# Optimization experiments

Hardware: AMD Instinct MI355X
Metric: run time of the kernel (lower is better)

Reference implementation:

```python
import math
import jax, jax.numpy as jnp
import numpy as np

B, S, DIM = 1, 1024, 2048
H, KVH, HD = 16, 4, 128
HID, L, VOCAB = 8192, 2, 32000
NIMG, TOK_START = 256, 1
IMG_IN = 2 * 14 * 14 * 3  # temporal_patch*spatial_patch^2*channels
EPS = 1e-6


def _rms(x, w=None, eps=EPS):
    y = x * jax.lax.rsqrt(jnp.mean(x * x, axis=-1, keepdims=True) + eps)
    return y if w is None else y * w


def _rope(x, angles):
    # x: [B,S,H,D], angles: [S, D//2] pairwise rotation angles (3D RoPE: 1D+2D concat)
    c = jnp.cos(angles)[None, :, None, :]
    s = jnp.sin(angles)[None, :, None, :]
    x1, x2 = x[..., 0::2], x[..., 1::2]
    return jnp.stack([x1 * c - x2 * s, x1 * s + x2 * c], axis=-1).reshape(x.shape)


def setup_inputs() -> dict:
    key = jax.random.key(0)
    ks = jax.random.split(key, 12)
    sc = 0.02
    return {
        "tokens": jax.random.randint(ks[0], (B, S), 0, VOCAB),
        "img_feats": jax.random.normal(ks[1], (B, NIMG, IMG_IN), jnp.float32),
        "freqs_cis": jax.random.normal(ks[2], (S, HD // 4), jnp.float32),
        "freqs_cis_2d": jax.random.normal(ks[3], (S, HD // 4), jnp.float32),
        "tok_emb": jax.random.normal(ks[4], (VOCAB, DIM), jnp.float32) * sc,
        "img_proj_w": jax.random.normal(ks[5], (DIM, IMG_IN), jnp.float32) * sc,
        "wqkv": jax.random.normal(ks[6], (L, H * HD + 2 * KVH * HD, DIM), jnp.float32) * sc,
        "wo": jax.random.normal(ks[7], (L, DIM, H * HD), jnp.float32) * sc,
        "sinks": jax.random.normal(ks[8], (L, H), jnp.float32),
        "w13": jax.random.normal(ks[9], (L, 2 * HID, DIM), jnp.float32) * sc,
        "w2": jax.random.normal(ks[10], (L, DIM, HID), jnp.float32) * sc,
        "norm_w": jnp.ones((DIM,), jnp.float32),
        "output_w": jax.random.normal(ks[11], (VOCAB, DIM), jnp.float32) * sc,
    }


def reference(tokens, img_feats, freqs_cis, freqs_cis_2d, tok_emb, img_proj_w,
              wqkv, wo, sinks, w13, w2, norm_w, output_w):
    # token embeddings + slice-based scatter of projected image tokens
    x = tok_emb[tokens]                                   # [B,S,DIM]
    img = jnp.einsum('bnf,df->bnd', img_feats, img_proj_w)
    x = jax.lax.dynamic_update_slice(x, img, (0, TOK_START, 0))

    angles = jnp.concatenate([freqs_cis, freqs_cis_2d], axis=-1)  # [S, HD//2]
    scale = 1.0 / math.sqrt(HD)
    neg = jnp.where(jnp.tril(jnp.ones((S, S), bool)), 0.0, -jnp.inf)  # causal
    n_rep = H // KVH
    q_dim, kv_dim = H * HD, KVH * HD

    for i in range(L):
        # attention: RMSNorm -> QKV -> QK-norm -> GQA expand -> RoPE -> SDPA+lse
        h = _rms(x)
        qkv = h @ wqkv[i].T
        q = qkv[..., :q_dim].reshape(B, S, H, HD)
        k = qkv[..., q_dim:q_dim + kv_dim].reshape(B, S, KVH, HD)
        v = qkv[..., q_dim + kv_dim:].reshape(B, S, KVH, HD)
        q, k = _rms(q), _rms(k)
        k = jnp.repeat(k, n_rep, axis=2)  # repeat_interleave over kv heads
        v = jnp.repeat(v, n_rep, axis=2)
        q, k = _rope(q, angles), _rope(k, angles)
        scores = jnp.einsum('bqhd,bkhd->bhqk', q, k) * scale + neg
        lse = jax.nn.logsumexp(scores, axis=-1)            # [B,H,S]
        attn = jnp.exp(scores - lse[..., None])
        out = jnp.einsum('bhqk,bkhd->bqhd', attn, v)        # [B,S,H,HD]
        sink_scale = jax.nn.sigmoid(lse - sinks[i][None, :, None])  # [B,H,S]
        out = out * sink_scale.transpose(0, 2, 1)[..., None]
        x = x + out.reshape(B, S, H * HD) @ wo[i].T

        # FFN: RMSNorm -> interleaved gate/up -> relu(gate)^2 * up -> down
        h = _rms(x)
        packed = h @ w13[i].T
        gate, up = packed[..., 0::2], packed[..., 1::2]
        x = x + (jnp.square(jax.nn.relu(gate)) * up) @ w2[i].T

    return _rms(x, norm_w) @ output_w.T                    # [B,S,VOCAB]
```

## Files before the change

kernel.cpp:

```cpp
#include <hip/hip_runtime.h>

typedef __bf16 bf16;
typedef bf16 bf16x8 __attribute__((ext_vector_type(8)));
typedef bf16 bf16x4 __attribute__((ext_vector_type(4)));
typedef bf16 bf16x2 __attribute__((ext_vector_type(2)));
typedef float f32x4 __attribute__((ext_vector_type(4)));
typedef float f32x2 __attribute__((ext_vector_type(2)));

#define S_LEN 1024
#define DIM 2048
#define NH 16
#define NKVH 4
#define HD 128
#define HID 8192
#define VOCAB 32000
#define QKV_N 3072
#define W13_N 16384
#define IMG_K 1176
#define NIMG 256

#define AS1 __attribute__((address_space(1)))
#define AS3 __attribute__((address_space(3)))

__device__ inline f32x4 mfma16(bf16x8 a, bf16x8 b, f32x4 c) {
  return __builtin_amdgcn_mfma_f32_16x16x32_bf16(a, b, c, 0, 0, 0);
}

__global__ void embed_kernel(const int* __restrict__ tok, const float* __restrict__ emb,
                             float* __restrict__ x) {
  int s = blockIdx.x, t = threadIdx.x;
  int id = tok[s];
  const float* er = emb + (size_t)id * DIM;
  float* xr = x + (size_t)s * DIM;
  *(f32x4*)(xr + t * 8)     = *(const f32x4*)(er + t * 8);
  *(f32x4*)(xr + t * 8 + 4) = *(const f32x4*)(er + t * 8 + 4);
}

__global__ void cvt_kernel(const float* __restrict__ in, bf16* __restrict__ o, int n) {
  int i = blockIdx.x * 256 + threadIdx.x;
  if (i < n) o[i] = (bf16)in[i];
}
__global__ void cvt4_kernel(const float* __restrict__ in, bf16* __restrict__ o, int n4) {
  int i = blockIdx.x * 256 + threadIdx.x;
  if (i < n4) {
    f32x4 v = *(const f32x4*)(in + (size_t)i * 4);
    bf16x4 b;
    b[0] = (bf16)v[0]; b[1] = (bf16)v[1]; b[2] = (bf16)v[2]; b[3] = (bf16)v[3];
    *(bf16x4*)(o + (size_t)i * 4) = b;
  }
}

template<int USE_W>
__global__ void rmsnorm_kernel(const float* __restrict__ x, const float* __restrict__ w,
                               bf16* __restrict__ o) {
  const int row = blockIdx.x, t = threadIdx.x;
  const float* xr = x + (size_t)row * DIM;
  f32x4 a = *(const f32x4*)(xr + t * 8);
  f32x4 b = *(const f32x4*)(xr + t * 8 + 4);
  float ss = a[0]*a[0] + a[1]*a[1] + a[2]*a[2] + a[3]*a[3]
           + b[0]*b[0] + b[1]*b[1] + b[2]*b[2] + b[3]*b[3];
#pragma unroll
  for (int off = 1; off < 64; off <<= 1) ss += __shfl_xor(ss, off);
  __shared__ float red[4];
  if ((t & 63) == 0) red[t >> 6] = ss;
  __syncthreads();
  ss = red[0] + red[1] + red[2] + red[3];
  float r = rsqrtf(ss * (1.0f / DIM) + 1e-6f);
  bf16x8 ov;
  if (USE_W) {
    f32x4 w1 = *(const f32x4*)(w + t * 8);
    f32x4 w2v = *(const f32x4*)(w + t * 8 + 4);
    ov[0] = (bf16)(a[0]*r*w1[0]); ov[1] = (bf16)(a[1]*r*w1[1]);
    ov[2] = (bf16)(a[2]*r*w1[2]); ov[3] = (bf16)(a[3]*r*w1[3]);
    ov[4] = (bf16)(b[0]*r*w2v[0]); ov[5] = (bf16)(b[1]*r*w2v[1]);
    ov[6] = (bf16)(b[2]*r*w2v[2]); ov[7] = (bf16)(b[3]*r*w2v[3]);
  } else {
    ov[0] = (bf16)(a[0]*r); ov[1] = (bf16)(a[1]*r);
    ov[2] = (bf16)(a[2]*r); ov[3] = (bf16)(a[3]*r);
    ov[4] = (bf16)(b[0]*r); ov[5] = (bf16)(b[1]*r);
    ov[6] = (bf16)(b[2]*r); ov[7] = (bf16)(b[3]*r);
  }
  *(bf16x8*)(o + (size_t)row * DIM + t * 8) = ov;
}

__global__ void qkvpost_kernel(const float* __restrict__ qkv, const float* __restrict__ f1,
                               const float* __restrict__ f2, bf16* __restrict__ qb,
                               bf16* __restrict__ kb, bf16* __restrict__ vtb) {
  int s = blockIdx.x, t = threadIdx.x;
  __shared__ float cs[64], sn[64];
  if (t < 64) {
    float ang = (t < 32) ? f1[(size_t)s * 32 + t] : f2[(size_t)s * 32 + (t - 32)];
    cs[t] = cosf(ang);
    sn[t] = sinf(ang);
  }
  __syncthreads();
  int w = t >> 6, lane = t & 63;
  for (int hh = w; hh < 24; hh += 4) {
    const float* base = qkv + (size_t)s * QKV_N + hh * HD;
    f32x2 e = *(const f32x2*)(base + lane * 2);
    if (hh < 20) {
      float ssum = e[0]*e[0] + e[1]*e[1];
#pragma unroll
      for (int off = 1; off < 64; off <<= 1) ssum += __shfl_xor(ssum, off);
      float r = rsqrtf(ssum * (1.0f / HD) + 1e-6f);
      float x1 = e[0] * r, x2 = e[1] * r;
      float c = cs[lane], s2 = sn[lane];
      bf16x2 ov;
      ov[0] = (bf16)(x1 * c - x2 * s2);
      ov[1] = (bf16)(x1 * s2 + x2 * c);
      if (hh < 16)
        *(bf16x2*)(qb + ((size_t)hh * S_LEN + s) * HD + lane * 2) = ov;
      else
        *(bf16x2*)(kb + ((size_t)(hh - 16) * S_LEN + s) * HD + lane * 2) = ov;
    } else {
      int kv = hh - 20;
      vtb[((size_t)kv * HD + lane * 2) * S_LEN + s]     = (bf16)e[0];
      vtb[((size_t)kv * HD + lane * 2 + 1) * S_LEN + s] = (bf16)e[1];
    }
  }
}

__global__ __launch_bounds__(256) void attn_kernel(const bf16* __restrict__ qb,
                                                   const bf16* __restrict__ kb,
                                                   const bf16* __restrict__ vtb,
                                                   const float* __restrict__ sinks,
                                                   bf16* __restrict__ out) {
  const int h = blockIdx.y, qs = blockIdx.x;
  const int w = threadIdx.x >> 6, lane = threadIdx.x & 63;
  const int lo = lane & 15, hi = lane >> 4;
  const int q0 = qs * 16;
  const int q = q0 + lo;
  const int kvh = h >> 2;
  const bf16* Q = qb + (size_t)h * S_LEN * HD;
  const bf16* Kp = kb + (size_t)kvh * S_LEN * HD;
  const bf16* Vt = vtb + (size_t)kvh * HD * S_LEN;
  const float scale = 0.08838834764831845f;

  __shared__ float accS[4][64 * 36];
  __shared__ float mS[4][16], lS[4][16];

  bf16x8 qf[4];
#pragma unroll
  for (int ks = 0; ks < 4; ++ks)
    qf[ks] = *(const bf16x8*)(Q + (size_t)q * HD + ks * 32 + hi * 8);

  f32x4 accT[8];
#pragma unroll
  for (int i = 0; i < 8; ++i) accT[i] = (f32x4){0.f, 0.f, 0.f, 0.f};
  float mrow = -3e38f, lrow = 0.f;

  const int nt = (q0 + 15) / 32 + 1;
  for (int tile = w; tile < nt; tile += 4) {
    const int kv0 = tile * 32;
    f32x4 st0 = (f32x4){0.f,0.f,0.f,0.f}, st1 = (f32x4){0.f,0.f,0.f,0.f};
#pragma unroll
    for (int ks = 0; ks < 4; ++ks) {
      const bf16* kbase = Kp + (size_t)(kv0 + lo) * HD + ks * 32 + hi * 8;
      bf16x8 k0f = *(const bf16x8*)(kbase);
      bf16x8 k1f = *(const bf16x8*)(kbase + 16 * HD);
      st0 = mfma16(k0f, qf[ks], st0);
      st1 = mfma16(k1f, qf[ks], st1);
    }
    float p[2][4];
    float pmax = -3e38f;
#pragma unroll
    for (int r = 0; r < 4; ++r) {
      int kvg0 = kv0 + hi * 4 + r;
      float v0 = (kvg0 <= q) ? st0[r] * scale : -3e38f;
      int kvg1 = kvg0 + 16;
      float v1 = (kvg1 <= q) ? st1[r] * scale : -3e38f;
      p[0][r] = v0; p[1][r] = v1;
      pmax = fmaxf(pmax, fmaxf(v0, v1));
    }
    pmax = fmaxf(pmax, __shfl_xor(pmax, 16));
    pmax = fmaxf(pmax, __shfl_xor(pmax, 32));
    float mnew = fmaxf(mrow, pmax);
    float alpha = __expf(mrow - mnew);
    float ps = 0.f;
#pragma unroll
    for (int f = 0; f < 2; ++f)
#pragma unroll
      for (int r = 0; r < 4; ++r) {
        float e = __expf(p[f][r] - mnew);
        p[f][r] = e;
        ps += e;
      }
    ps += __shfl_xor(ps, 16);
    ps += __shfl_xor(ps, 32);
    lrow = lrow * alpha + ps;
    mrow = mnew;
#pragma unroll
    for (int fd = 0; fd < 8; ++fd) {
      accT[fd][0] *= alpha; accT[fd][1] *= alpha;
      accT[fd][2] *= alpha; accT[fd][3] *= alpha;
    }
    bf16x8 pb;
#pragma unroll
    for (int j = 0; j < 8; ++j) {
      int src = ((j >> 2) + 2 * (hi & 1)) * 16 + lo;
      float v0 = __shfl(p[0][j & 3], src);
      float v1 = __shfl(p[1][j & 3], src);
      pb[j] = (bf16)((hi >= 2) ? v1 : v0);
    }
#pragma unroll
    for (int fd = 0; fd < 8; ++fd) {
      bf16x8 vf = *(const bf16x8*)(Vt + (size_t)(fd * 16 + lo) * S_LEN + kv0 + hi * 8);
      accT[fd] = mfma16(vf, pb, accT[fd]);
    }
  }
  if (hi == 0) { mS[w][lo] = mrow; lS[w][lo] = lrow; }
  float* as = &accS[w][lane * 36];
#pragma unroll
  for (int fd = 0; fd < 8; ++fd) *(f32x4*)(as + fd * 4) = accT[fd];
  __syncthreads();
  float m0 = mS[0][lo], m1 = mS[1][lo], m2 = mS[2][lo], m3 = mS[3][lo];
  float mstar = fmaxf(fmaxf(m0, m1), fmaxf(m2, m3));
  float e0 = __expf(m0 - mstar), e1 = __expf(m1 - mstar);
  float e2 = __expf(m2 - mstar), e3 = __expf(m3 - mstar);
  float lstar = lS[0][lo]*e0 + lS[1][lo]*e1 + lS[2][lo]*e2 + lS[3][lo]*e3;
  float lse = mstar + __logf(lstar);
  float ssig = 1.f / (1.f + __expf(sinks[h] - lse));
  float sc = ssig / lstar;
#pragma unroll
  for (int f2 = 0; f2 < 2; ++f2) {
    int fd = w * 2 + f2;
    f32x4 a0 = *(const f32x4*)&accS[0][lane * 36 + fd * 4];
    f32x4 a1 = *(const f32x4*)&accS[1][lane * 36 + fd * 4];
    f32x4 a2 = *(const f32x4*)&accS[2][lane * 36 + fd * 4];
    f32x4 a3 = *(const f32x4*)&accS[3][lane * 36 + fd * 4];
#pragma unroll
    for (int r = 0; r < 4; ++r) {
      float o = a0[r]*e0 + a1[r]*e1 + a2[r]*e2 + a3[r]*e3;
      out[(size_t)q * DIM + h * HD + fd * 16 + hi * 4 + r] = (bf16)(o * sc);
    }
  }
}

__device__ inline void xcd_remap(int ntm, int ntn, int& mtile, int& ntile) {
  const int flat = blockIdx.x + ntm * blockIdx.y;
  const int chunk = ntm * 8;
  const int gfull = ntn >> 3;
  const int g = flat / chunk;
  if (g < gfull) {
    int rem = flat - g * chunk;
    ntile = g * 8 + (rem & 7);
    mtile = rem >> 3;
  } else {
    int rem = flat - gfull * chunk;
    int nrem = ntn - gfull * 8;
    ntile = gfull * 8 + rem % nrem;
    mtile = rem / nrem;
  }
}

enum { EPI_STORE = 0, EPI_ADD = 1, EPI_ACT = 2 };

template<int BM, int BN, int EPI, int GL>
__global__ void gemm_bt(const bf16* __restrict__ A, const float* __restrict__ W,
                        float* __restrict__ C, bf16* __restrict__ Cb,
                        int M, int N, int K, int ldc) {
  constexpr int BK = 64;
  __shared__ __align__(16) char lds[(BM + BN) * BK * 2];
  char* ldsA = lds;
  char* ldsB = lds + BM * BK * 2;
  const int t = threadIdx.x;
  int mtile, ntile;
  xcd_remap(gridDim.x, gridDim.y, mtile, ntile);
  const int m0 = mtile * BM, n0 = ntile * BN;

  const int wid = t >> 6, lane = t & 63;
  const int lo = lane & 15, hi = lane >> 4;
  const int wr = wid >> 1, wc = wid & 1;
  constexpr int TM = BM / 32, TN = BN / 32;
  constexpr int NA = BM / 32;
  constexpr int NPASS = BM / 32;
  constexpr int NW = BN / 16;

  f32x4 acc[TM][TN];
#pragma unroll
  for (int m = 0; m < TM; ++m)
#pragma unroll
    for (int n = 0; n < TN; ++n) acc[m][n] = (f32x4){0.f, 0.f, 0.f, 0.f};

  const int nk = (K + BK - 1) / BK;
  for (int kt = 0; kt < nk; ++kt) {
    const int k0 = kt * BK;
    bf16x8 av[NA];
    f32x4 wv[NW];
    if (!GL) {
#pragma unroll
      for (int i = 0; i < NA; ++i) {
        int c = t + i * 256;
        int row = c >> 3, kc = c & 7;
        int kg = k0 + kc * 8;
        bf16x8 z = {};
        av[i] = (kg < K) ? *(const bf16x8*)(A + (size_t)(m0 + row) * K + kg) : z;
      }
    }
#pragma unroll
    for (int i = 0; i < NW; ++i) {
      int c = t + i * 256;
      int row = c >> 4, kc = c & 15;
      int kg = k0 + kc * 4;
      f32x4 z = (f32x4){0.f, 0.f, 0.f, 0.f};
      wv[i] = (kg < K) ? *(const f32x4*)(W + (size_t)(n0 + row) * K + kg) : z;
    }
    __syncthreads();
    if (GL) {
#pragma unroll
      for (int i = 0; i < NPASS; ++i) {
        int row = i * 32 + (t >> 3);
        int srcb = ((t & 7) * 16) ^ ((row & 7) << 4);
        const bf16* g2 = A + (size_t)(m0 + row) * K + k0 + (srcb >> 1);
        char* l = ldsA + i * 4096 + wid * 1024;
        __builtin_amdgcn_global_load_lds((const AS1 void*)g2, (AS3 void*)l, 16, 0, 0);
      }
    } else {
#pragma unroll
      for (int i = 0; i < NA; ++i) {
        int c = t + i * 256;
        int row = c >> 3, kc = c & 7;
        int kb = (kc * 16) ^ ((row & 7) << 4);
        *(bf16x8*)(ldsA + row * 128 + kb) = av[i];
      }
    }
#pragma unroll
    for (int i = 0; i < NW; ++i) {
      int c = t + i * 256;
      int row = c >> 4, kc = c & 15;
      bf16x4 bv;
      bv[0] = (bf16)wv[i][0]; bv[1] = (bf16)wv[i][1];
      bv[2] = (bf16)wv[i][2]; bv[3] = (bf16)wv[i][3];
      int kb = (kc * 8) ^ ((row & 7) << 4);
      *(bf16x4*)(ldsB + row * 128 + kb) = bv;
    }
    __syncthreads();
#pragma unroll
    for (int ks = 0; ks < 2; ++ks) {
      bf16x8 af[TM], bfr[TN];
      int kbb = ks * 64 + hi * 16;
#pragma unroll
      for (int m = 0; m < TM; ++m) {
        int row = wr * (BM / 2) + m * 16 + lo;
        af[m] = *(const bf16x8*)(ldsA + row * 128 + (kbb ^ ((row & 7) << 4)));
      }
#pragma unroll
      for (int n = 0; n < TN; ++n) {
        int row = wc * (BN / 2) + n * 16 + lo;
        bfr[n] = *(const bf16x8*)(ldsB + row * 128 + (kbb ^ ((row & 7) << 4)));
      }
#pragma unroll
      for (int m = 0; m < TM; ++m)
#pragma unroll
        for (int n = 0; n < TN; ++n)
          acc[m][n] = mfma16(af[m], bfr[n], acc[m][n]);
    }
    __syncthreads();
  }
#pragma unroll
  for (int m = 0; m < TM; ++m) {
    int gmb = m0 + wr * (BM / 2) + m * 16 + hi * 4;
#pragma unroll
    for (int n = 0; n < TN; ++n) {
      int gn = n0 + wc * (BN / 2) + n * 16 + lo;
#pragma unroll
      for (int r = 0; r < 4; ++r) {
        float v = acc[m][n][r];
        if (EPI == EPI_STORE) {
          C[(size_t)(gmb + r) * ldc + gn] = v;
        } else if (EPI == EPI_ADD) {
          C[(size_t)(gmb + r) * ldc + gn] += v;
        } else {
          float pv = __shfl_xor(v, 1);
          if (!(lane & 1)) {
            float g2 = fmaxf(v, 0.f);
            Cb[(size_t)(gmb + r) * (W13_N / 2) + (gn >> 1)] = (bf16)(g2 * g2 * pv);
          }
        }
      }
    }
  }
}

template<int BM, int BN, int EPI>
__global__ __launch_bounds__(256) void gemm_bb(const bf16* __restrict__ A,
                                               const bf16* __restrict__ W,
                                               float* __restrict__ C, bf16* __restrict__ Cb,
                                               int K, int ldc) {
  constexpr int BK = 64;
  __shared__ __align__(16) char lds[(BM + BN) * BK * 2];
  char* ldsA = lds;
  char* ldsB = lds + BM * BK * 2;
  const int t = threadIdx.x;
  int mtile, ntile;
  xcd_remap(gridDim.x, gridDim.y, mtile, ntile);
  const int m0 = mtile * BM, n0 = ntile * BN;

  const int wid = t >> 6, lane = t & 63;
  const int lo = lane & 15, hi = lane >> 4;
  const int wr = wid >> 1, wc = wid & 1;
  constexpr int TM = BM / 32, TN = BN / 32;
  constexpr int PA = BM / 32, PB = BN / 32;

  f32x4 acc[TM][TN];
#pragma unroll
  for (int m = 0; m < TM; ++m)
#pragma unroll
    for (int n = 0; n < TN; ++n) acc[m][n] = (f32x4){0.f, 0.f, 0.f, 0.f};

  const int prow = t >> 3;
  const int psrcb = (t & 7) * 16;
  const int nk = K / BK;
  for (int kt = 0; kt < nk; ++kt) {
    const int k0 = kt * BK;
#pragma unroll
    for (int i = 0; i < PA; ++i) {
      int row = i * 32 + prow;
      int srcb = psrcb ^ ((row & 7) << 4);
      const bf16* g = A + (size_t)(m0 + row) * K + k0 + (srcb >> 1);
      __builtin_amdgcn_global_load_lds((const AS1 void*)g,
                                       (AS3 void*)(ldsA + i * 4096 + wid * 1024), 16, 0, 0);
    }
#pragma unroll
    for (int i = 0; i < PB; ++i) {
      int row = i * 32 + prow;
      int srcb = psrcb ^ ((row & 7) << 4);
      const bf16* g = W + (size_t)(n0 + row) * K + k0 + (srcb >> 1);
      __builtin_amdgcn_global_load_lds((const AS1 void*)g,
                                       (AS3 void*)(ldsB + i * 4096 + wid * 1024), 16, 0, 0);
    }
    __syncthreads();
#pragma unroll
    for (int ks = 0; ks < 2; ++ks) {
      bf16x8 af[TM], bfr[TN];
      int kbb = ks * 64 + hi * 16;
#pragma unroll
      for (int m = 0; m < TM; ++m) {
        int row = wr * (BM / 2) + m * 16 + lo;
        af[m] = *(const bf16x8*)(ldsA + row * 128 + (kbb ^ ((row & 7) << 4)));
      }
#pragma unroll
      for (int n = 0; n < TN; ++n) {
        int row = wc * (BN / 2) + n * 16 + lo;
        bfr[n] = *(const bf16x8*)(ldsB + row * 128 + (kbb ^ ((row & 7) << 4)));
      }
#pragma unroll
      for (int m = 0; m < TM; ++m)
#pragma unroll
        for (int n = 0; n < TN; ++n)
          acc[m][n] = mfma16(af[m], bfr[n], acc[m][n]);
    }
    __syncthreads();
  }
#pragma unroll
  for (int m = 0; m < TM; ++m) {
    int gmb = m0 + wr * (BM / 2) + m * 16 + hi * 4;
#pragma unroll
    for (int n = 0; n < TN; ++n) {
      int gn = n0 + wc * (BN / 2) + n * 16 + lo;
#pragma unroll
      for (int r = 0; r < 4; ++r) {
        float v = acc[m][n][r];
        if (EPI == EPI_STORE) {
          C[(size_t)(gmb + r) * ldc + gn] = v;
        } else if (EPI == EPI_ADD) {
          C[(size_t)(gmb + r) * ldc + gn] += v;
        } else {
          float pv = __shfl_xor(v, 1);
          if (!(lane & 1)) {
            float g2 = fmaxf(v, 0.f);
            Cb[(size_t)(gmb + r) * (W13_N / 2) + (gn >> 1)] = (bf16)(g2 * g2 * pv);
          }
        }
      }
    }
  }
}

template<int EPI>
__global__ __launch_bounds__(512, 1) void gemm_2pf(const bf16* __restrict__ A,
                                                   const float* __restrict__ W,
                                                   float* __restrict__ C, bf16* __restrict__ Cb,
                                                   int K, int ldc) {
  extern __shared__ __align__(16) char lds[];
  char* ldsA = lds;
  char* ldsB = lds + 65536;
  const int t = threadIdx.x;
  int mtile, ntile;
  xcd_remap(gridDim.x, gridDim.y, mtile, ntile);
  const int m0 = mtile * 256, n0 = ntile * 256;
  const int wid = t >> 6, lane = t & 63;
  const int lo = lane & 15, hi = lane >> 4;
  const int wr = wid >> 2, wc = wid & 3;

  f32x4 acc[8][4];
#pragma unroll
  for (int f = 0; f < 8; ++f)
#pragma unroll
    for (int g = 0; g < 4; ++g) acc[f][g] = (f32x4){0.f, 0.f, 0.f, 0.f};

  const int prow = t >> 3;
  const int pcol = (t & 7) * 16;

  auto STAGEA = [&](int h, int kt2) {
    char* dst = ldsA + (kt2 & 1) * 32768 + h * 16384;
    const int k0 = kt2 * 64;
#pragma unroll
    for (int i = 0; i < 2; ++i) {
      int row = i * 64 + prow;
      int srcb = pcol ^ ((row & 7) << 4);
      const bf16* g = A + (size_t)(m0 + h * 128 + row) * K + k0 + (srcb >> 1);
      __builtin_amdgcn_global_load_lds((const AS1 void*)g,
          (AS3 void*)(dst + i * 8192 + wid * 1024), 16, 0, 0);
    }
  };

  f32x4 breg[4][2];
  auto BLOAD = [&](int kt2) {
#pragma unroll
    for (int i = 0; i < 4; ++i) {
      int c = t + i * 512;
      int row = c >> 3, kc = c & 7;
      const float* g = W + (size_t)(n0 + row) * K + kt2 * 64 + kc * 8;
      breg[i][0] = *(const f32x4*)(g);
      breg[i][1] = *(const f32x4*)(g + 4);
    }
  };
  auto BWRITE = [&](int kt2) {
#pragma unroll
    for (int i = 0; i < 4; ++i) {
      int c = t + i * 512;
      int row = c >> 3, kc = c & 7;
      int h = row >> 7, rowh = row & 127;
      bf16x8 bv;
#pragma unroll
      for (int e = 0; e < 4; ++e) {
        bv[e]     = (bf16)breg[i][0][e];
        bv[4 + e] = (bf16)breg[i][1][e];
      }
      *(bf16x8*)(ldsB + (kt2 & 1) * 32768 + h * 16384 + rowh * 128 +
                 ((kc * 16) ^ ((rowh & 7) << 4))) = bv;
    }
  };

  auto LDA = [&](int buf, int mh, int i, int ks) -> bf16x8 {
    int row = (mh * 4 + i) * 16 + lo;
    return *(const bf16x8*)(ldsA + buf * 32768 + wr * 16384 + row * 128 +
                            ((ks * 64 + hi * 16) ^ ((row & 7) << 4)));
  };
  auto LDB = [&](int buf, int nh, int j, int ks) -> bf16x8 {
    int rowh = (wc & 1) * 64 + (nh * 2 + j) * 16 + lo;
    return *(const bf16x8*)(ldsB + buf * 32768 + (wc >> 1) * 16384 + rowh * 128 +
                            ((ks * 64 + hi * 16) ^ ((rowh & 7) << 4)));
  };

  const int nk = K / 64;
  STAGEA(0, 0);
  STAGEA(1, 0);
  __builtin_amdgcn_sched_barrier(0);
  BLOAD(0);
  __builtin_amdgcn_sched_barrier(0);
  asm volatile("s_waitcnt vmcnt(8)" ::: "memory");
  __builtin_amdgcn_s_barrier();
  asm volatile("" ::: "memory");

  for (int kt = 0; kt < nk; ++kt) {
    const int buf = kt & 1;
    const bool more = (kt + 1) < nk;
    BWRITE(kt);
    asm volatile("s_waitcnt lgkmcnt(0)" ::: "memory");
    __builtin_amdgcn_s_barrier();
    asm volatile("" ::: "memory");
    if (more) {
      STAGEA(0, kt + 1);
      STAGEA(1, kt + 1);
      __builtin_amdgcn_sched_barrier(0);
      BLOAD(kt + 1);
      __builtin_amdgcn_sched_barrier(0);
    }
#pragma unroll
    for (int mh = 0; mh < 2; ++mh) {
      bf16x8 a[4][2];
#pragma unroll
      for (int i = 0; i < 4; ++i) { a[i][0] = LDA(buf, mh, i, 0); a[i][1] = LDA(buf, mh, i, 1); }
#pragma unroll
      for (int nh = 0; nh < 2; ++nh) {
        bf16x8 b[2][2];
#pragma unroll
        for (int j = 0; j < 2; ++j) { b[j][0] = LDB(buf, nh, j, 0); b[j][1] = LDB(buf, nh, j, 1); }
        __builtin_amdgcn_s_setprio(1);
#pragma unroll
        for (int i = 0; i < 4; ++i)
#pragma unroll
          for (int j = 0; j < 2; ++j) {
            acc[mh * 4 + i][nh * 2 + j] = mfma16(a[i][0], b[j][0], acc[mh * 4 + i][nh * 2 + j]);
            acc[mh * 4 + i][nh * 2 + j] = mfma16(a[i][1], b[j][1], acc[mh * 4 + i][nh * 2 + j]);
          }
        __builtin_amdgcn_s_setprio(0);
      }
    }
    if (more) asm volatile("s_waitcnt vmcnt(8)" ::: "memory");
    else      asm volatile("s_waitcnt vmcnt(0)" ::: "memory");
    __builtin_amdgcn_s_barrier();
    asm volatile("" ::: "memory");
  }
#pragma unroll
  for (int f = 0; f < 8; ++f) {
    int gmb = m0 + wr * 128 + f * 16 + hi * 4;
#pragma unroll
    for (int g = 0; g < 4; ++g) {
      int gn = n0 + wc * 64 + g * 16 + lo;
#pragma unroll
      for (int r = 0; r < 4; ++r) {
        float v = acc[f][g][r];
        if (EPI == EPI_STORE) {
          C[(size_t)(gmb + r) * ldc + gn] = v;
        } else if (EPI == EPI_ADD) {
          C[(size_t)(gmb + r) * ldc + gn] += v;
        } else {
          float pv = __shfl_xor(v, 1);
          if (!(lane & 1)) {
            float g2 = fmaxf(v, 0.f);
            Cb[(size_t)(gmb + r) * (W13_N / 2) + (gn >> 1)] = (bf16)(g2 * g2 * pv);
          }
        }
      }
    }
  }
}

extern "C" void kernel_launch(void* const* d_in, const int* in_sizes, int n_in,
                              void* d_out, int out_size, void* d_ws, size_t ws_size,
                              hipStream_t stream) {
  const int* tokens = (const int*)d_in[0];
  const float* img_feats = (const float*)d_in[1];
  const float* freqs = (const float*)d_in[2];
  const float* freqs2 = (const float*)d_in[3];
  const float* tok_emb = (const float*)d_in[4];
  const float* img_proj_w = (const float*)d_in[5];
  const float* wqkv = (const float*)d_in[6];
  const float* wo = (const float*)d_in[7];
  const float* sinks = (const float*)d_in[8];
  const float* w13 = (const float*)d_in[9];
  const float* w2 = (const float*)d_in[10];
  const float* norm_w = (const float*)d_in[11];
  const float* output_w = (const float*)d_in[12];
  float* out = (float*)d_out;

  char* ws = (char*)d_ws;
  float* x = (float*)ws;   ws += (size_t)S_LEN * DIM * 4;
  bf16* h = (bf16*)ws;     ws += (size_t)S_LEN * DIM * 2;
  float* qkv = (float*)ws; ws += (size_t)S_LEN * QKV_N * 4;
  bf16* qb = (bf16*)ws;    ws += (size_t)NH * S_LEN * HD * 2;
  bf16* kb = (bf16*)ws;    ws += (size_t)NKVH * S_LEN * HD * 2;
  bf16* vtb = (bf16*)ws;   ws += (size_t)NKVH * HD * S_LEN * 2;
  bf16* ao = (bf16*)ws;    ws += (size_t)S_LEN * DIM * 2;
  bf16* act = (bf16*)ws;   ws += (size_t)S_LEN * HID * 2;
  bf16* imgb = (bf16*)ws;  ws += (size_t)NIMG * IMG_K * 2;
  const size_t n_wqkv = (size_t)2 * QKV_N * DIM;
  const size_t n_wo   = (size_t)2 * DIM * (NH * HD);
  const size_t n_w2   = (size_t)2 * DIM * HID;
  bf16* wqkvb = (bf16*)ws; ws += n_wqkv * 2;
  bf16* wob   = (bf16*)ws; ws += n_wo * 2;
  bf16* w2b   = (bf16*)ws; ws += n_w2 * 2;
  const bool bf16_path = ((size_t)(ws - (char*)d_ws) <= ws_size);

  bool big_ok = false;
  {
    hipError_t e1 = hipFuncSetAttribute((const void*)&gemm_2pf<EPI_STORE>,
                                        hipFuncAttributeMaxDynamicSharedMemorySize, 131072);
    hipError_t e2 = hipFuncSetAttribute((const void*)&gemm_2pf<EPI_ACT>,
                                        hipFuncAttributeMaxDynamicSharedMemorySize, 131072);
    if (e1 == hipSuccess && e2 == hipSuccess) {
      hipFuncAttributes fa1{}, fa2{};
      if (hipFuncGetAttributes(&fa1, (const void*)&gemm_2pf<EPI_STORE>) == hipSuccess &&
          hipFuncGetAttributes(&fa2, (const void*)&gemm_2pf<EPI_ACT>) == hipSuccess)
        big_ok = fa1.maxDynamicSharedSizeBytes >= 131072 &&
                 fa2.maxDynamicSharedSizeBytes >= 131072;
    }
  }

  embed_kernel<<<S_LEN, 256, 0, stream>>>(tokens, tok_emb, x);
  cvt_kernel<<<(NIMG * IMG_K + 255) / 256, 256, 0, stream>>>(img_feats, imgb, NIMG * IMG_K);
  gemm_bt<64, 128, EPI_STORE, 0><<<dim3(NIMG / 64, DIM / 128), 256, 0, stream>>>(
      imgb, img_proj_w, x + DIM, nullptr, NIMG, DIM, IMG_K, DIM);

  if (bf16_path) {
    cvt4_kernel<<<(int)(n_wqkv / 4 + 255) / 256, 256, 0, stream>>>(wqkv, wqkvb, (int)(n_wqkv / 4));
    cvt4_kernel<<<(int)(n_wo / 4 + 255) / 256, 256, 0, stream>>>(wo, wob, (int)(n_wo / 4));
    cvt4_kernel<<<(int)(n_w2 / 4 + 255) / 256, 256, 0, stream>>>(w2, w2b, (int)(n_w2 / 4));
  }

  for (int i = 0; i < 2; ++i) {
    rmsnorm_kernel<0><<<S_LEN, 256, 0, stream>>>(x, nullptr, h);
    if (bf16_path) {
      gemm_bb<64, 128, EPI_STORE><<<dim3(S_LEN / 64, QKV_N / 128), 256, 0, stream>>>(
          h, wqkvb + (size_t)i * QKV_N * DIM, qkv, nullptr, DIM, QKV_N);
    } else {
      gemm_bt<64, 128, EPI_STORE, 1><<<dim3(S_LEN / 64, QKV_N / 128), 256, 0, stream>>>(
          h, wqkv + (size_t)i * QKV_N * DIM, qkv, nullptr, S_LEN, QKV_N, DIM, QKV_N);
    }
    qkvpost_kernel<<<S_LEN, 256, 0, stream>>>(qkv, freqs, freqs2, qb, kb, vtb);
    attn_kernel<<<dim3(S_LEN / 16, NH), 256, 0, stream>>>(qb, kb, vtb, sinks + i * NH, ao);
    if (bf16_path) {
      gemm_bb<64, 128, EPI_ADD><<<dim3(S_LEN / 64, DIM / 128), 256, 0, stream>>>(
          ao, wob + (size_t)i * DIM * DIM, x, nullptr, DIM, DIM);
    } else {
      gemm_bt<64, 128, EPI_ADD, 1><<<dim3(S_LEN / 64, DIM / 128), 256, 0, stream>>>(
          ao, wo + (size_t)i * DIM * DIM, x, nullptr, S_LEN, DIM, DIM, DIM);
    }
    rmsnorm_kernel<0><<<S_LEN, 256, 0, stream>>>(x, nullptr, h);
    if (big_ok) {
      gemm_2pf<EPI_ACT><<<dim3(S_LEN / 256, W13_N / 256), 512, 131072, stream>>>(
          h, w13 + (size_t)i * W13_N * DIM, nullptr, act, DIM, 0);
    } else {
      gemm_bt<128, 128, EPI_ACT, 1><<<dim3(S_LEN / 128, W13_N / 128), 256, 0, stream>>>(
          h, w13 + (size_t)i * W13_N * DIM, nullptr, act, S_LEN, W13_N, DIM, 0);
    }
    if (bf16_path) {
      gemm_bb<64, 128, EPI_ADD><<<dim3(S_LEN / 64, DIM / 128), 256, 0, stream>>>(
          act, w2b + (size_t)i * DIM * HID, x, nullptr, HID, DIM);
    } else {
      gemm_bt<64, 128, EPI_ADD, 1><<<dim3(S_LEN / 64, DIM / 128), 256, 0, stream>>>(
          act, w2 + (size_t)i * DIM * HID, x, nullptr, S_LEN, DIM, HID, DIM);
    }
  }
  rmsnorm_kernel<1><<<S_LEN, 256, 0, stream>>>(x, norm_w, h);
  if (big_ok) {
    gemm_2pf<EPI_STORE><<<dim3(S_LEN / 256, VOCAB / 256), 512, 131072, stream>>>(
        h, output_w, out, nullptr, DIM, VOCAB);
  } else {
    gemm_bt<128, 128, EPI_STORE, 1><<<dim3(S_LEN / 128, VOCAB / 128), 256, 0, stream>>>(
        h, output_w, out, nullptr, S_LEN, VOCAB, DIM, VOCAB);
  }
}
```

Before: 1.031 ms.

## Split-K wo/w2 GEMMs with atomic accumulation and widen attention KV tiles to 64

The wo and w2 residual-add GEMMs now split the K dimension in two across blockIdx.z and accumulate into x with atomicAdd. This doubles the number of workgroups (16x16 = 256 becomes 512) so the GPU is better filled. Separately, the attention kernel now processes 64 KV positions per iteration instead of 32, which halves the per-tile softmax and rescale overhead. The costs are atomic traffic, nondeterministic summation order, and higher register pressure in the attention kernel.

```diff
diff --git a/kernel.cpp b/kernel.cpp
--- a/kernel.cpp
+++ b/kernel.cpp
@@ -149,36 +149,39 @@
   for (int i = 0; i < 8; ++i) accT[i] = (f32x4){0.f, 0.f, 0.f, 0.f};
   float mrow = -3e38f, lrow = 0.f;
 
-  const int nt = (q0 + 15) / 32 + 1;
-  for (int tile = w; tile < nt; tile += 4) {
-    const int kv0 = tile * 32;
-    f32x4 st0 = (f32x4){0.f,0.f,0.f,0.f}, st1 = (f32x4){0.f,0.f,0.f,0.f};
+  const int ntc = (q0 + 15) / 64 + 1;
+  for (int c = w; c < ntc; c += 4) {
+    const int kv0 = c * 64;
+    f32x4 st[4];
+#pragma unroll
+    for (int f = 0; f < 4; ++f) st[f] = (f32x4){0.f, 0.f, 0.f, 0.f};
 #pragma unroll
     for (int ks = 0; ks < 4; ++ks) {
       const bf16* kbase = Kp + (size_t)(kv0 + lo) * HD + ks * 32 + hi * 8;
-      bf16x8 k0f = *(const bf16x8*)(kbase);
-      bf16x8 k1f = *(const bf16x8*)(kbase + 16 * HD);
-      st0 = mfma16(k0f, qf[ks], st0);
-      st1 = mfma16(k1f, qf[ks], st1);
-    }
-    float p[2][4];
+#pragma unroll
+      for (int f = 0; f < 4; ++f) {
+        bf16x8 kf = *(const bf16x8*)(kbase + (size_t)f * 16 * HD);
+        st[f] = mfma16(kf, qf[ks], st[f]);
+      }
+    }
+    float p[4][4];
     float pmax = -3e38f;
 #pragma unroll
-    for (int r = 0; r < 4; ++r) {
-      int kvg0 = kv0 + hi * 4 + r;
-      float v0 = (kvg0 <= q) ? st0[r] * scale : -3e38f;
-      int kvg1 = kvg0 + 16;
-      float v1 = (kvg1 <= q) ? st1[r] * scale : -3e38f;
-      p[0][r] = v0; p[1][r] = v1;
-      pmax = fmaxf(pmax, fmaxf(v0, v1));
-    }
+    for (int f = 0; f < 4; ++f)
+#pragma unroll
+      for (int r = 0; r < 4; ++r) {
+        int kvg = kv0 + f * 16 + hi * 4 + r;
+        float v = (kvg <= q) ? st[f][r] * scale : -3e38f;
+        p[f][r] = v;
+        pmax = fmaxf(pmax, v);
+      }
     pmax = fmaxf(pmax, __shfl_xor(pmax, 16));
     pmax = fmaxf(pmax, __shfl_xor(pmax, 32));
     float mnew = fmaxf(mrow, pmax);
     float alpha = __expf(mrow - mnew);
     float ps = 0.f;
 #pragma unroll
-    for (int f = 0; f < 2; ++f)
+    for (int f = 0; f < 4; ++f)
 #pragma unroll
       for (int r = 0; r < 4; ++r) {
         float e = __expf(p[f][r] - mnew);
@@ -194,18 +197,24 @@
       accT[fd][0] *= alpha; accT[fd][1] *= alpha;
       accT[fd][2] *= alpha; accT[fd][3] *= alpha;
     }
-    bf16x8 pb;
+    bf16x8 pb0, pb1;
 #pragma unroll
     for (int j = 0; j < 8; ++j) {
       int src = ((j >> 2) + 2 * (hi & 1)) * 16 + lo;
       float v0 = __shfl(p[0][j & 3], src);
       float v1 = __shfl(p[1][j & 3], src);
-      pb[j] = (bf16)((hi >= 2) ? v1 : v0);
+      pb0[j] = (bf16)((hi >= 2) ? v1 : v0);
+      float v2 = __shfl(p[2][j & 3], src);
+      float v3 = __shfl(p[3][j & 3], src);
+      pb1[j] = (bf16)((hi >= 2) ? v3 : v2);
     }
 #pragma unroll
     for (int fd = 0; fd < 8; ++fd) {
-      bf16x8 vf = *(const bf16x8*)(Vt + (size_t)(fd * 16 + lo) * S_LEN + kv0 + hi * 8);
-      accT[fd] = mfma16(vf, pb, accT[fd]);
+      const bf16* vrow = Vt + (size_t)(fd * 16 + lo) * S_LEN + kv0 + hi * 8;
+      bf16x8 vf0 = *(const bf16x8*)(vrow);
+      bf16x8 vf1 = *(const bf16x8*)(vrow + 32);
+      accT[fd] = mfma16(vf0, pb0, accT[fd]);
+      accT[fd] = mfma16(vf1, pb1, accT[fd]);
     }
   }
   if (hi == 0) { mS[w][lo] = mrow; lS[w][lo] = lrow; }
@@ -253,7 +262,7 @@
   }
 }
 
-enum { EPI_STORE = 0, EPI_ADD = 1, EPI_ACT = 2 };
+enum { EPI_STORE = 0, EPI_ADD = 1, EPI_ACT = 2, EPI_ADDA = 3 };
 
 template<int BM, int BN, int EPI, int GL>
 __global__ void gemm_bt(const bf16* __restrict__ A, const float* __restrict__ W,
@@ -386,7 +395,7 @@
 __global__ __launch_bounds__(256) void gemm_bb(const bf16* __restrict__ A,
                                                const bf16* __restrict__ W,
                                                float* __restrict__ C, bf16* __restrict__ Cb,
-                                               int K, int ldc) {
+                                               int strideK, int kLen, int ldc) {
   constexpr int BK = 64;
   __shared__ __align__(16) char lds[(BM + BN) * BK * 2];
   char* ldsA = lds;
@@ -395,6 +404,7 @@
   int mtile, ntile;
   xcd_remap(gridDim.x, gridDim.y, mtile, ntile);
   const int m0 = mtile * BM, n0 = ntile * BN;
+  const int koff = blockIdx.z * kLen;
 
   const int wid = t >> 6, lane = t & 63;
   const int lo = lane & 15, hi = lane >> 4;
@@ -410,14 +420,14 @@
 
   const int prow = t >> 3;
   const int psrcb = (t & 7) * 16;
-  const int nk = K / BK;
+  const int nk = kLen / BK;
   for (int kt = 0; kt < nk; ++kt) {
-    const int k0 = kt * BK;
+    const int k0 = koff + kt * BK;
 #pragma unroll
     for (int i = 0; i < PA; ++i) {
       int row = i * 32 + prow;
       int srcb = psrcb ^ ((row & 7) << 4);
-      const bf16* g = A + (size_t)(m0 + row) * K + k0 + (srcb >> 1);
+      const bf16* g = A + (size_t)(m0 + row) * strideK + k0 + (srcb >> 1);
       __builtin_amdgcn_global_load_lds((const AS1 void*)g,
                                        (AS3 void*)(ldsA + i * 4096 + wid * 1024), 16, 0, 0);
     }
@@ -425,7 +435,7 @@
     for (int i = 0; i < PB; ++i) {
       int row = i * 32 + prow;
       int srcb = psrcb ^ ((row & 7) << 4);
-      const bf16* g = W + (size_t)(n0 + row) * K + k0 + (srcb >> 1);
+      const bf16* g = W + (size_t)(n0 + row) * strideK + k0 + (srcb >> 1);
       __builtin_amdgcn_global_load_lds((const AS1 void*)g,
                                        (AS3 void*)(ldsB + i * 4096 + wid * 1024), 16, 0, 0);
     }
@@ -465,6 +475,8 @@
           C[(size_t)(gmb + r) * ldc + gn] = v;
         } else if (EPI == EPI_ADD) {
           C[(size_t)(gmb + r) * ldc + gn] += v;
+        } else if (EPI == EPI_ADDA) {
+          atomicAdd(&C[(size_t)(gmb + r) * ldc + gn], v);
         } else {
           float pv = __shfl_xor(v, 1);
           if (!(lane & 1)) {
@@ -694,8 +706,8 @@
   for (int i = 0; i < 2; ++i) {
     rmsnorm_kernel<0><<<S_LEN, 256, 0, stream>>>(x, nullptr, h);
     if (bf16_path) {
-      gemm_bb<64, 128, EPI_STORE><<<dim3(S_LEN / 64, QKV_N / 128), 256, 0, stream>>>(
-          h, wqkvb + (size_t)i * QKV_N * DIM, qkv, nullptr, DIM, QKV_N);
+      gemm_bb<64, 128, EPI_STORE><<<dim3(S_LEN / 64, QKV_N / 128, 1), 256, 0, stream>>>(
+          h, wqkvb + (size_t)i * QKV_N * DIM, qkv, nullptr, DIM, DIM, QKV_N);
     } else {
       gemm_bt<64, 128, EPI_STORE, 1><<<dim3(S_LEN / 64, QKV_N / 128), 256, 0, stream>>>(
           h, wqkv + (size_t)i * QKV_N * DIM, qkv, nullptr, S_LEN, QKV_N, DIM, QKV_N);
@@ -703,8 +715,8 @@
     qkvpost_kernel<<<S_LEN, 256, 0, stream>>>(qkv, freqs, freqs2, qb, kb, vtb);
     attn_kernel<<<dim3(S_LEN / 16, NH), 256, 0, stream>>>(qb, kb, vtb, sinks + i * NH, ao);
     if (bf16_path) {
-      gemm_bb<64, 128, EPI_ADD><<<dim3(S_LEN / 64, DIM / 128), 256, 0, stream>>>(
-          ao, wob + (size_t)i * DIM * DIM, x, nullptr, DIM, DIM);
+      gemm_bb<64, 128, EPI_ADDA><<<dim3(S_LEN / 64, DIM / 128, 2), 256, 0, stream>>>(
+          ao, wob + (size_t)i * DIM * DIM, x, nullptr, DIM, DIM / 2, DIM);
     } else {
       gemm_bt<64, 128, EPI_ADD, 1><<<dim3(S_LEN / 64, DIM / 128), 256, 0, stream>>>(
           ao, wo + (size_t)i * DIM * DIM, x, nullptr, S_LEN, DIM, DIM, DIM);
@@ -718,8 +730,8 @@
           h, w13 + (size_t)i * W13_N * DIM, nullptr, act, S_LEN, W13_N, DIM, 0);
     }
     if (bf16_path) {
-      gemm_bb<64, 128, EPI_ADD><<<dim3(S_LEN / 64, DIM / 128), 256, 0, stream>>>(
-          act, w2b + (size_t)i * DIM * HID, x, nullptr, HID, DIM);
+      gemm_bb<64, 128, EPI_ADDA><<<dim3(S_LEN / 64, DIM / 128, 2), 256, 0, stream>>>(
+          act, w2b + (size_t)i * DIM * HID, x, nullptr, HID, HID / 2, DIM);
     } else {
       gemm_bt<64, 128, EPI_ADD, 1><<<dim3(S_LEN / 64, DIM / 128), 256, 0, stream>>>(
           act, w2 + (size_t)i * DIM * HID, x, nullptr, S_LEN, DIM, HID, DIM);
```

New measurement: 894.5 us. 1.15x faster.
